# Kernel optimization log

Measured on AMD Instinct MI355X. Metric: run time of the kernel, lower is better.

## Reference

```python
import jax, jax.numpy as jnp
import numpy as np

DIM = 640
M_SPATIAL = 100  # 10*10
BATCH = 64
EPS = 1e-5


def setup_inputs() -> dict:
    key = jax.random.key(0)
    kx, = jax.random.split(key, 1)
    x = jax.random.normal(kx, (BATCH, DIM, M_SPATIAL), dtype=jnp.float32)
    # temperature buffer: log(1 / (2 * H * W)) as in BDC.__init__
    t = jnp.log(1.0 / (2.0 * M_SPATIAL) * jnp.ones((1, 1), dtype=jnp.float32))
    return {"x": x, "t": t}


def reference(x, t):
    B, dim, M = x.shape
    # x_pow2 = x @ x^T  -> [B, dim, dim]
    x_pow2 = jnp.einsum('bim,bjm->bij', x, x)
    # I_M.bmm(x_pow2*I) broadcasts diag along rows; (x_pow2*I).bmm(I_M) along cols
    d = jnp.diagonal(x_pow2, axis1=1, axis2=2)  # [B, dim], squared norms
    dcov = d[:, :, None] + d[:, None, :] - 2.0 * x_pow2
    dcov = jnp.clip(dcov, 0.0)
    dcov = jnp.exp(t) * dcov
    dcov = jnp.sqrt(dcov + EPS)
    # double centering: dcov.bmm(I_M) = row sums broadcast, I_M.bmm(dcov) = col sums
    row_mean = jnp.sum(dcov, axis=2, keepdims=True) / dim          # [B, dim, 1]
    col_mean = jnp.sum(dcov, axis=1, keepdims=True) / dim          # [B, 1, dim]
    grand_mean = jnp.sum(dcov, axis=(1, 2), keepdims=True) / (dim * dim)
    bdc = dcov - row_mean - col_mean + grand_mean                   # [B, dim, dim]
    # Triuvec: upper triangle incl. diagonal, row-major order
    iu_r, iu_c = np.triu_indices(dim)
    return bdc[:, iu_r, iu_c]  # [B, dim*(dim+1)//2]
```

## Files before the change

kernel.cpp:

```cpp
#include <hip/hip_runtime.h>
#include <math.h>

#define BATCH 64
#define DIM   640
#define MSP   100
#define TILE  64
#define NT    10
#define NPAIR 55
#define PTRI  205120
#define EPSV  1e-5f

#define WS_D 0
#define WS_S 40960
#define WS_G 81920
#define XB_OFF 327936ull
#define TI_OFF 10813696ull


typedef __attribute__((ext_vector_type(8))) short short8;
typedef __attribute__((ext_vector_type(4))) float f32x4;
typedef __attribute__((ext_vector_type(2))) __fp16 fp16x2;

__device__ __forceinline__ short f2bf(float f) {
    union { float f; unsigned u; } x; x.f = f;
    unsigned r = x.u + 0x7fffu + ((x.u >> 16) & 1u);
    return (short)(r >> 16);
}
__device__ __forceinline__ float bf2f(short h) {
    union { unsigned u; float f; } x; x.u = ((unsigned)(unsigned short)h) << 16;
    return x.f;
}

__device__ __forceinline__ void decode_pair(int u, int& ti, int& tj) {
    ti = 0;
    while (u >= NT - ti) { u -= NT - ti; ++ti; }
    tj = ti + u;
}

__global__ __launch_bounds__(256) void k_prep(const float* __restrict__ x,
                                              float* __restrict__ ws) {
    short* xb = (short*)((char*)ws + XB_OFF);
    const int t = threadIdx.x;
    const int rr = t >> 4, c = t & 15;
    const int row = blockIdx.x * 16 + rr;
    const int k0 = c * 8;
    const float* src = x + (size_t)row * MSP;

    float v[8];
#pragma unroll
    for (int e = 0; e < 8; ++e) v[e] = 0.f;
    if (k0 <= 88) {
        float4 u0 = *(const float4*)(src + k0);
        float4 u1 = *(const float4*)(src + k0 + 4);
        v[0] = u0.x; v[1] = u0.y; v[2] = u0.z; v[3] = u0.w;
        v[4] = u1.x; v[5] = u1.y; v[6] = u1.z; v[7] = u1.w;
    } else if (k0 == 96) {
        float4 u0 = *(const float4*)(src + 96);
        v[0] = u0.x; v[1] = u0.y; v[2] = u0.z; v[3] = u0.w;
    }

    short8 h; float s = 0.f;
#pragma unroll
    for (int e = 0; e < 8; ++e) {
        short hb = f2bf(v[e]);
        float vr = bf2f(hb);
        s += vr * vr;
        h[e] = hb;
    }
    *(short8*)(xb + (size_t)blockIdx.x * 2048 + c * 128 + rr * 8) = h;

    s += __shfl_xor(s, 1); s += __shfl_xor(s, 2);
    s += __shfl_xor(s, 4); s += __shfl_xor(s, 8);
    if (c == 0) { ws[WS_D + row] = s; ws[WS_S + row] = 0.f; }
    if (blockIdx.x == 0 && t < BATCH) ws[WS_G + t] = 0.f;
}

__global__ __launch_bounds__(256) void k_gram(const float* __restrict__ tsc,
                                              float* __restrict__ ws) {
    __shared__ float sRow[TILE];
    __shared__ float sCol[TILE];

    int ti, tj;
    decode_pair(blockIdx.x, ti, tj);
    const int b = blockIdx.y;
    const int i0 = ti * TILE, j0 = tj * TILE;
    const int tid = threadIdx.x;
    const short* xb = (const short*)((const char*)ws + XB_OFF);

    if (tid < TILE) { sRow[tid] = 0.f; sCol[tid] = 0.f; }

    const int wave = tid >> 6, lane = tid & 63;
    const int lm = lane & 15, lq = lane >> 4;
    const int r0 = (wave >> 1) * 32, c0 = (wave & 1) * 32;

    const short* pa = xb + (size_t)(b * 40 + ((i0 + r0) >> 4)) * 2048 + lq * 128 + lm * 8;
    const short* pb = xb + (size_t)(b * 40 + ((j0 + c0) >> 4)) * 2048 + lq * 128 + lm * 8;

    f32x4 acc[2][2] = {};
#pragma unroll
    for (int ks = 0; ks < 4; ++ks) {
        short8 a0 = *(const short8*)(pa + ks * 512);
        short8 a1 = *(const short8*)(pa + 2048 + ks * 512);
        short8 b0 = *(const short8*)(pb + ks * 512);
        short8 b1 = *(const short8*)(pb + 2048 + ks * 512);
        acc[0][0] = __builtin_amdgcn_mfma_f32_16x16x32_bf16(a0, b0, acc[0][0], 0, 0, 0);
        acc[0][1] = __builtin_amdgcn_mfma_f32_16x16x32_bf16(a0, b1, acc[0][1], 0, 0, 0);
        acc[1][0] = __builtin_amdgcn_mfma_f32_16x16x32_bf16(a1, b0, acc[1][0], 0, 0, 0);
        acc[1][1] = __builtin_amdgcn_mfma_f32_16x16x32_bf16(a1, b1, acc[1][1], 0, 0, 0);
    }

    const float scale = expf(tsc[0]);
    const float* dn = ws + WS_D + b * DIM;
    float di[2][4], dj[2];
#pragma unroll
    for (int a = 0; a < 2; ++a)
#pragma unroll
        for (int r = 0; r < 4; ++r) di[a][r] = dn[i0 + r0 + 16 * a + lq * 4 + r];
#pragma unroll
    for (int bb = 0; bb < 2; ++bb) dj[bb] = dn[j0 + c0 + 16 * bb + lm];

    float rp[2][4] = {}, cp[2] = {};
    short* tb = (short*)((char*)ws + TI_OFF) + ((size_t)(b * NPAIR + blockIdx.x) << 12);
    uint4 st[2];
#pragma unroll
    for (int a = 0; a < 2; ++a) {
        unsigned wd[4];
#pragma unroll
        for (int bb = 0; bb < 2; ++bb)
#pragma unroll
            for (int p = 0; p < 2; ++p) {
                float d0 = di[a][2 * p]     + dj[bb];
                float d1 = di[a][2 * p + 1] + dj[bb];
                float v0 = __builtin_amdgcn_sqrtf(
                    fmaf(scale, fmaxf(fmaf(-2.f, acc[a][bb][2 * p],     d0), 0.f), EPSV));
                float v1 = __builtin_amdgcn_sqrtf(
                    fmaf(scale, fmaxf(fmaf(-2.f, acc[a][bb][2 * p + 1], d1), 0.f), EPSV));
                rp[a][2 * p] += v0; rp[a][2 * p + 1] += v1; cp[bb] += v0 + v1;
                union { fp16x2 h; unsigned u; } cv;
                cv.h = __builtin_amdgcn_cvt_pkrtz(v0, v1);
                wd[bb * 2 + p] = cv.u;
            }
        st[a].x = wd[0]; st[a].y = wd[1]; st[a].z = wd[2]; st[a].w = wd[3];
    }
    *(uint4*)(tb + tid * 16)     = st[0];
    *(uint4*)(tb + tid * 16 + 8) = st[1];

    __syncthreads();
#pragma unroll
    for (int a = 0; a < 2; ++a)
#pragma unroll
        for (int r = 0; r < 4; ++r) {
            float v = rp[a][r];
            v += __shfl_xor(v, 1); v += __shfl_xor(v, 2);
            v += __shfl_xor(v, 4); v += __shfl_xor(v, 8);
            if (lm == 0) atomicAdd(&sRow[r0 + 16 * a + lq * 4 + r], v);
        }
#pragma unroll
    for (int bb = 0; bb < 2; ++bb) {
        float v = cp[bb];
        v += __shfl_xor(v, 16); v += __shfl_xor(v, 32);
        if (lq == 0) atomicAdd(&sCol[c0 + 16 * bb + lm], v);
    }
    __syncthreads();

    float* S = ws + WS_S + b * DIM;
    if (tid < TILE) {
        atomicAdd(&S[i0 + tid], sRow[tid]);
        if (ti != tj) atomicAdd(&S[j0 + tid], sCol[tid]);
        float gg = sRow[tid];
        gg += __shfl_xor(gg, 1);  gg += __shfl_xor(gg, 2);  gg += __shfl_xor(gg, 4);
        gg += __shfl_xor(gg, 8);  gg += __shfl_xor(gg, 16); gg += __shfl_xor(gg, 32);
        if (tid == 0) atomicAdd(&ws[WS_G + b], (ti == tj ? 1.f : 2.f) * gg);
    }
}

__global__ __launch_bounds__(256) void k_final(const float* __restrict__ ws,
                                               float* __restrict__ out) {
    int ti, tj;
    decode_pair(blockIdx.x, ti, tj);
    const int b = blockIdx.y;
    const int i0 = ti * TILE, j0 = tj * TILE;
    const int tid = threadIdx.x;
    const int wave = tid >> 6, lane = tid & 63;
    const int lm = lane & 15, lq = lane >> 4;
    const int r0 = (wave >> 1) * 32, c0 = (wave & 1) * 32;

    const uint4* tb = (const uint4*)((const char*)ws + TI_OFF +
                                     ((size_t)(b * NPAIR + blockIdx.x) << 13));
    uint4 u[2];
    u[0] = tb[tid * 2]; u[1] = tb[tid * 2 + 1];

    const float inv = 1.f / (float)DIM;
    const float g = ws[WS_G + b] * (inv * inv);
    const float* S = ws + WS_S + b * DIM;

    float ai[2][4]; int ib[2][4];
#pragma unroll
    for (int a = 0; a < 2; ++a)
#pragma unroll
        for (int r = 0; r < 4; ++r) {
            int i = i0 + r0 + 16 * a + 4 * lq + r;
            ai[a][r] = g - S[i] * inv;
            ib[a][r] = i * DIM - (i * (i - 1)) / 2 - i;
        }
    float bj[2]; int jj[2];
#pragma unroll
    for (int bb = 0; bb < 2; ++bb) {
        int j = j0 + c0 + 16 * bb + lm;
        jj[bb] = j; bj[bb] = -S[j] * inv;
    }

    const bool offd = (ti != tj);
    float* outb = out + (size_t)b * PTRI;
#pragma unroll
    for (int a = 0; a < 2; ++a) {
        unsigned wd[4] = {u[a].x, u[a].y, u[a].z, u[a].w};
        const int ibase = i0 + r0 + 16 * a + 4 * lq;
#pragma unroll
        for (int bb = 0; bb < 2; ++bb)
#pragma unroll
            for (int p = 0; p < 2; ++p) {
                union { unsigned u; fp16x2 h; } cv; cv.u = wd[bb * 2 + p];
                float v0 = (float)cv.h.x, v1 = (float)cv.h.y;
                const int r = 2 * p;
                if (offd || jj[bb] >= ibase + r)
                    outb[ib[a][r] + jj[bb]] = v0 + ai[a][r] + bj[bb];
                if (offd || jj[bb] >= ibase + r + 1)
                    outb[ib[a][r + 1] + jj[bb]] = v1 + ai[a][r + 1] + bj[bb];
            }
    }
}

extern "C" void kernel_launch(void* const* d_in, const int* in_sizes, int n_in,
                              void* d_out, int out_size, void* d_ws, size_t ws_size,
                              hipStream_t stream) {
    const float* x = (const float*)d_in[0];
    const float* t = (const float*)d_in[1];
    float* out = (float*)d_out;
    float* ws  = (float*)d_ws;

    k_prep <<<dim3(BATCH * DIM / 16), 256, 0, stream>>>(x, ws);
    k_gram <<<dim3(NPAIR, BATCH),     256, 0, stream>>>(t, ws);
    k_final<<<dim3(NPAIR, BATCH),     256, 0, stream>>>(ws, out);
}
```

Baseline: 130.5 us.

## Fuse gram and finalize kernels with grid barrier, keep tiles in registers

```diff
diff --git a/kernel.cpp b/kernel.cpp
--- a/kernel.cpp
+++ b/kernel.cpp
@@ -9,12 +9,14 @@
 #define NPAIR 55
 #define PTRI  205120
 #define EPSV  1e-5f
+#define GRID  440
+#define TPB   8
 
 #define WS_D 0
 #define WS_S 40960
 #define WS_G 81920
-#define XB_OFF 327936ull
-#define TI_OFF 10813696ull
+#define WS_C 81984
+#define XB_OFF 328192ull
 
 
 typedef __attribute__((ext_vector_type(8))) short short8;
@@ -30,7 +32,6 @@
     union { unsigned u; float f; } x; x.u = ((unsigned)(unsigned short)h) << 16;
     return x.f;
 }
-
 __device__ __forceinline__ void decode_pair(int u, int& ti, int& tj) {
     ti = 0;
     while (u >= NT - ti) { u -= NT - ti; ++ti; }
@@ -41,9 +42,9 @@
                                               float* __restrict__ ws) {
     short* xb = (short*)((char*)ws + XB_OFF);
     const int t = threadIdx.x;
-    const int rr = t >> 4, c = t & 15;
+    const int rr = t >> 4, cc = t & 15;
     const int row = blockIdx.x * 16 + rr;
-    const int k0 = c * 8;
+    const int k0 = cc * 8;
     const float* src = x + (size_t)row * MSP;
 
     float v[8];
@@ -67,167 +68,170 @@
         s += vr * vr;
         h[e] = hb;
     }
-    *(short8*)(xb + (size_t)blockIdx.x * 2048 + c * 128 + rr * 8) = h;
+    *(short8*)(xb + (size_t)blockIdx.x * 2048 + cc * 128 + rr * 8) = h;
 
     s += __shfl_xor(s, 1); s += __shfl_xor(s, 2);
     s += __shfl_xor(s, 4); s += __shfl_xor(s, 8);
-    if (c == 0) { ws[WS_D + row] = s; ws[WS_S + row] = 0.f; }
-    if (blockIdx.x == 0 && t < BATCH) ws[WS_G + t] = 0.f;
-}
-
-__global__ __launch_bounds__(256) void k_gram(const float* __restrict__ tsc,
-                                              float* __restrict__ ws) {
-    __shared__ float sRow[TILE];
-    __shared__ float sCol[TILE];
-
-    int ti, tj;
-    decode_pair(blockIdx.x, ti, tj);
-    const int b = blockIdx.y;
-    const int i0 = ti * TILE, j0 = tj * TILE;
+    if (cc == 0) ws[WS_D + row] = s;
+}
+
+__device__ __forceinline__ void grid_barrier(unsigned* cnt, int tid) {
+    __syncthreads();
+    if (tid == 0) {
+        __threadfence();
+        atomicAdd(cnt, 1u);
+        while (__hip_atomic_load(cnt, __ATOMIC_ACQUIRE, __HIP_MEMORY_SCOPE_AGENT) < GRID)
+            __builtin_amdgcn_s_sleep(2);
+        __threadfence();
+    }
+    __syncthreads();
+}
+
+__global__ __launch_bounds__(256, 2) void k_fused(const float* __restrict__ tsc,
+                                                  float* __restrict__ ws,
+                                                  float* __restrict__ out) {
+    short* xb = (short*)((char*)ws + XB_OFF);
     const int tid = threadIdx.x;
-    const short* xb = (const short*)((const char*)ws + XB_OFF);
-
-    if (tid < TILE) { sRow[tid] = 0.f; sCol[tid] = 0.f; }
-
+
+    const float scale = expf(tsc[0]);
     const int wave = tid >> 6, lane = tid & 63;
     const int lm = lane & 15, lq = lane >> 4;
     const int r0 = (wave >> 1) * 32, c0 = (wave & 1) * 32;
-
-    const short* pa = xb + (size_t)(b * 40 + ((i0 + r0) >> 4)) * 2048 + lq * 128 + lm * 8;
-    const short* pb = xb + (size_t)(b * 40 + ((j0 + c0) >> 4)) * 2048 + lq * 128 + lm * 8;
-
-    f32x4 acc[2][2] = {};
-#pragma unroll
-    for (int ks = 0; ks < 4; ++ks) {
-        short8 a0 = *(const short8*)(pa + ks * 512);
-        short8 a1 = *(const short8*)(pa + 2048 + ks * 512);
-        short8 b0 = *(const short8*)(pb + ks * 512);
-        short8 b1 = *(const short8*)(pb + 2048 + ks * 512);
-        acc[0][0] = __builtin_amdgcn_mfma_f32_16x16x32_bf16(a0, b0, acc[0][0], 0, 0, 0);
-        acc[0][1] = __builtin_amdgcn_mfma_f32_16x16x32_bf16(a0, b1, acc[0][1], 0, 0, 0);
-        acc[1][0] = __builtin_amdgcn_mfma_f32_16x16x32_bf16(a1, b0, acc[1][0], 0, 0, 0);
-        acc[1][1] = __builtin_amdgcn_mfma_f32_16x16x32_bf16(a1, b1, acc[1][1], 0, 0, 0);
-    }
-
-    const float scale = expf(tsc[0]);
-    const float* dn = ws + WS_D + b * DIM;
-    float di[2][4], dj[2];
-#pragma unroll
-    for (int a = 0; a < 2; ++a)
-#pragma unroll
-        for (int r = 0; r < 4; ++r) di[a][r] = dn[i0 + r0 + 16 * a + lq * 4 + r];
-#pragma unroll
-    for (int bb = 0; bb < 2; ++bb) dj[bb] = dn[j0 + c0 + 16 * bb + lm];
-
-    float rp[2][4] = {}, cp[2] = {};
-    short* tb = (short*)((char*)ws + TI_OFF) + ((size_t)(b * NPAIR + blockIdx.x) << 12);
-    uint4 st[2];
-#pragma unroll
-    for (int a = 0; a < 2; ++a) {
-        unsigned wd[4];
-#pragma unroll
-        for (int bb = 0; bb < 2; ++bb)
-#pragma unroll
-            for (int p = 0; p < 2; ++p) {
-                float d0 = di[a][2 * p]     + dj[bb];
-                float d1 = di[a][2 * p + 1] + dj[bb];
-                float v0 = __builtin_amdgcn_sqrtf(
-                    fmaf(scale, fmaxf(fmaf(-2.f, acc[a][bb][2 * p],     d0), 0.f), EPSV));
-                float v1 = __builtin_amdgcn_sqrtf(
-                    fmaf(scale, fmaxf(fmaf(-2.f, acc[a][bb][2 * p + 1], d1), 0.f), EPSV));
-                rp[a][2 * p] += v0; rp[a][2 * p + 1] += v1; cp[bb] += v0 + v1;
-                union { fp16x2 h; unsigned u; } cv;
-                cv.h = __builtin_amdgcn_cvt_pkrtz(v0, v1);
-                wd[bb * 2 + p] = cv.u;
+    const int tbase = blockIdx.x * TPB;
+
+    uint4 tr[TPB][2];
+
+#pragma unroll
+    for (int s8 = 0; s8 < TPB; ++s8) {
+        const int u = tbase + s8;
+        const int b = u / NPAIR;
+        int ti, tj;
+        decode_pair(u - b * NPAIR, ti, tj);
+        const int i0 = ti * TILE, j0 = tj * TILE;
+        const float* dn = ws + WS_D + b * DIM;
+        float* S = ws + WS_S + b * DIM;
+
+        const short* pa = xb + (size_t)(b * 40 + ((i0 + r0) >> 4)) * 2048 + lq * 128 + lm * 8;
+        const short* pb = xb + (size_t)(b * 40 + ((j0 + c0) >> 4)) * 2048 + lq * 128 + lm * 8;
+
+        f32x4 acc[2][2] = {};
+#pragma unroll
+        for (int ks = 0; ks < 4; ++ks) {
+            short8 a0 = *(const short8*)(pa + ks * 512);
+            short8 a1 = *(const short8*)(pa + 2048 + ks * 512);
+            short8 b0 = *(const short8*)(pb + ks * 512);
+            short8 b1 = *(const short8*)(pb + 2048 + ks * 512);
+            acc[0][0] = __builtin_amdgcn_mfma_f32_16x16x32_bf16(a0, b0, acc[0][0], 0, 0, 0);
+            acc[0][1] = __builtin_amdgcn_mfma_f32_16x16x32_bf16(a0, b1, acc[0][1], 0, 0, 0);
+            acc[1][0] = __builtin_amdgcn_mfma_f32_16x16x32_bf16(a1, b0, acc[1][0], 0, 0, 0);
+            acc[1][1] = __builtin_amdgcn_mfma_f32_16x16x32_bf16(a1, b1, acc[1][1], 0, 0, 0);
+        }
+
+        float di[2][4], dj[2];
+#pragma unroll
+        for (int a = 0; a < 2; ++a)
+#pragma unroll
+            for (int r = 0; r < 4; ++r) di[a][r] = dn[i0 + r0 + 16 * a + lq * 4 + r];
+#pragma unroll
+        for (int bb = 0; bb < 2; ++bb) dj[bb] = dn[j0 + c0 + 16 * bb + lm];
+
+        float rp[2][4] = {}, cp[2] = {};
+#pragma unroll
+        for (int a = 0; a < 2; ++a) {
+            unsigned wd[4];
+#pragma unroll
+            for (int bb = 0; bb < 2; ++bb)
+#pragma unroll
+                for (int p = 0; p < 2; ++p) {
+                    float d0 = di[a][2 * p]     + dj[bb];
+                    float d1 = di[a][2 * p + 1] + dj[bb];
+                    float v0 = __builtin_amdgcn_sqrtf(
+                        fmaf(scale, fmaxf(fmaf(-2.f, acc[a][bb][2 * p],     d0), 0.f), EPSV));
+                    float v1 = __builtin_amdgcn_sqrtf(
+                        fmaf(scale, fmaxf(fmaf(-2.f, acc[a][bb][2 * p + 1], d1), 0.f), EPSV));
+                    rp[a][2 * p] += v0; rp[a][2 * p + 1] += v1; cp[bb] += v0 + v1;
+                    union { fp16x2 h; unsigned u; } cv;
+                    cv.h = __builtin_amdgcn_cvt_pkrtz(v0, v1);
+                    wd[bb * 2 + p] = cv.u;
+                }
+            tr[s8][a].x = wd[0]; tr[s8][a].y = wd[1];
+            tr[s8][a].z = wd[2]; tr[s8][a].w = wd[3];
+        }
+
+        float tsum = 0.f;
+#pragma unroll
+        for (int a = 0; a < 2; ++a)
+#pragma unroll
+            for (int r = 0; r < 4; ++r) {
+                float v = rp[a][r];
+                tsum += v;
+                v += __shfl_xor(v, 1); v += __shfl_xor(v, 2);
+                v += __shfl_xor(v, 4); v += __shfl_xor(v, 8);
+                if (lm == 0) atomicAdd(&S[i0 + r0 + 16 * a + lq * 4 + r], v);
             }
-        st[a].x = wd[0]; st[a].y = wd[1]; st[a].z = wd[2]; st[a].w = wd[3];
-    }
-    *(uint4*)(tb + tid * 16)     = st[0];
-    *(uint4*)(tb + tid * 16 + 8) = st[1];
-
-    __syncthreads();
-#pragma unroll
-    for (int a = 0; a < 2; ++a)
-#pragma unroll
-        for (int r = 0; r < 4; ++r) {
-            float v = rp[a][r];
-            v += __shfl_xor(v, 1); v += __shfl_xor(v, 2);
-            v += __shfl_xor(v, 4); v += __shfl_xor(v, 8);
-            if (lm == 0) atomicAdd(&sRow[r0 + 16 * a + lq * 4 + r], v);
-        }
-#pragma unroll
-    for (int bb = 0; bb < 2; ++bb) {
-        float v = cp[bb];
-        v += __shfl_xor(v, 16); v += __shfl_xor(v, 32);
-        if (lq == 0) atomicAdd(&sCol[c0 + 16 * bb + lm], v);
-    }
-    __syncthreads();
-
-    float* S = ws + WS_S + b * DIM;
-    if (tid < TILE) {
-        atomicAdd(&S[i0 + tid], sRow[tid]);
-        if (ti != tj) atomicAdd(&S[j0 + tid], sCol[tid]);
-        float gg = sRow[tid];
-        gg += __shfl_xor(gg, 1);  gg += __shfl_xor(gg, 2);  gg += __shfl_xor(gg, 4);
-        gg += __shfl_xor(gg, 8);  gg += __shfl_xor(gg, 16); gg += __shfl_xor(gg, 32);
-        if (tid == 0) atomicAdd(&ws[WS_G + b], (ti == tj ? 1.f : 2.f) * gg);
-    }
-}
-
-__global__ __launch_bounds__(256) void k_final(const float* __restrict__ ws,
-                                               float* __restrict__ out) {
-    int ti, tj;
-    decode_pair(blockIdx.x, ti, tj);
-    const int b = blockIdx.y;
-    const int i0 = ti * TILE, j0 = tj * TILE;
-    const int tid = threadIdx.x;
-    const int wave = tid >> 6, lane = tid & 63;
-    const int lm = lane & 15, lq = lane >> 4;
-    const int r0 = (wave >> 1) * 32, c0 = (wave & 1) * 32;
-
-    const uint4* tb = (const uint4*)((const char*)ws + TI_OFF +
-                                     ((size_t)(b * NPAIR + blockIdx.x) << 13));
-    uint4 u[2];
-    u[0] = tb[tid * 2]; u[1] = tb[tid * 2 + 1];
+        if (ti != tj) {
+#pragma unroll
+            for (int bb = 0; bb < 2; ++bb) {
+                float v = cp[bb];
+                v += __shfl_xor(v, 16); v += __shfl_xor(v, 32);
+                if (lq == 0) atomicAdd(&S[j0 + c0 + 16 * bb + lm], v);
+            }
+        }
+        tsum += __shfl_xor(tsum, 1);  tsum += __shfl_xor(tsum, 2);
+        tsum += __shfl_xor(tsum, 4);  tsum += __shfl_xor(tsum, 8);
+        tsum += __shfl_xor(tsum, 16); tsum += __shfl_xor(tsum, 32);
+        if (lane == 0) atomicAdd(&ws[WS_G + b], (ti == tj ? 1.f : 2.f) * tsum);
+    }
+
+    grid_barrier((unsigned*)(ws + WS_C), tid);
 
     const float inv = 1.f / (float)DIM;
-    const float g = ws[WS_G + b] * (inv * inv);
-    const float* S = ws + WS_S + b * DIM;
-
-    float ai[2][4]; int ib[2][4];
-#pragma unroll
-    for (int a = 0; a < 2; ++a)
-#pragma unroll
-        for (int r = 0; r < 4; ++r) {
-            int i = i0 + r0 + 16 * a + 4 * lq + r;
-            ai[a][r] = g - S[i] * inv;
-            ib[a][r] = i * DIM - (i * (i - 1)) / 2 - i;
-        }
-    float bj[2]; int jj[2];
-#pragma unroll
-    for (int bb = 0; bb < 2; ++bb) {
-        int j = j0 + c0 + 16 * bb + lm;
-        jj[bb] = j; bj[bb] = -S[j] * inv;
-    }
-
-    const bool offd = (ti != tj);
-    float* outb = out + (size_t)b * PTRI;
-#pragma unroll
-    for (int a = 0; a < 2; ++a) {
-        unsigned wd[4] = {u[a].x, u[a].y, u[a].z, u[a].w};
-        const int ibase = i0 + r0 + 16 * a + 4 * lq;
-#pragma unroll
-        for (int bb = 0; bb < 2; ++bb)
-#pragma unroll
-            for (int p = 0; p < 2; ++p) {
-                union { unsigned u; fp16x2 h; } cv; cv.u = wd[bb * 2 + p];
-                float v0 = (float)cv.h.x, v1 = (float)cv.h.y;
-                const int r = 2 * p;
-                if (offd || jj[bb] >= ibase + r)
-                    outb[ib[a][r] + jj[bb]] = v0 + ai[a][r] + bj[bb];
-                if (offd || jj[bb] >= ibase + r + 1)
-                    outb[ib[a][r + 1] + jj[bb]] = v1 + ai[a][r + 1] + bj[bb];
+
+#pragma unroll
+    for (int s8 = 0; s8 < TPB; ++s8) {
+        const int u = tbase + s8;
+        const int b = u / NPAIR;
+        int ti, tj;
+        decode_pair(u - b * NPAIR, ti, tj);
+        const int i0 = ti * TILE, j0 = tj * TILE;
+        const bool offd = (ti != tj);
+        const float* S = ws + WS_S + b * DIM;
+        const float g = ws[WS_G + b] * (inv * inv);
+        float* outb = out + (size_t)b * PTRI;
+
+        float ai[2][4]; int ib[2][4];
+#pragma unroll
+        for (int a = 0; a < 2; ++a)
+#pragma unroll
+            for (int r = 0; r < 4; ++r) {
+                int i = i0 + r0 + 16 * a + 4 * lq + r;
+                ai[a][r] = g - S[i] * inv;
+                ib[a][r] = i * DIM - (i * (i - 1)) / 2 - i;
             }
+        float bj[2]; int jj[2];
+#pragma unroll
+        for (int bb = 0; bb < 2; ++bb) {
+            int j = j0 + c0 + 16 * bb + lm;
+            jj[bb] = j; bj[bb] = -S[j] * inv;
+        }
+
+#pragma unroll
+        for (int a = 0; a < 2; ++a) {
+            unsigned wd[4] = {tr[s8][a].x, tr[s8][a].y, tr[s8][a].z, tr[s8][a].w};
+            const int ibase = i0 + r0 + 16 * a + 4 * lq;
+#pragma unroll
+            for (int bb = 0; bb < 2; ++bb)
+#pragma unroll
+                for (int p = 0; p < 2; ++p) {
+                    union { unsigned uu; fp16x2 h; } cv; cv.uu = wd[bb * 2 + p];
+                    float v0 = (float)cv.h.x, v1 = (float)cv.h.y;
+                    const int r = 2 * p;
+                    if (offd || jj[bb] >= ibase + r)
+                        outb[ib[a][r] + jj[bb]] = v0 + ai[a][r] + bj[bb];
+                    if (offd || jj[bb] >= ibase + r + 1)
+                        outb[ib[a][r + 1] + jj[bb]] = v1 + ai[a][r + 1] + bj[bb];
+                }
+        }
     }
 }
 
@@ -239,7 +243,8 @@
     float* out = (float*)d_out;
     float* ws  = (float*)d_ws;
 
+    hipMemsetAsync((char*)ws + (size_t)WS_S * 4, 0,
+                   (size_t)(DIM * BATCH + BATCH + 16) * 4, stream);
     k_prep <<<dim3(BATCH * DIM / 16), 256, 0, stream>>>(x, ws);
-    k_gram <<<dim3(NPAIR, BATCH),     256, 0, stream>>>(t, ws);
-    k_final<<<dim3(NPAIR, BATCH),     256, 0, stream>>>(ws, out);
-}
+    k_fused<<<dim3(GRID),             256, 0, stream>>>(t, ws, out);
+}
```

Result: slower. 239.9 us (+83.8%).
